# Optimization experiments

Hardware: AMD Instinct MI355X
Metric: run time of the kernel (lower is better)

The kernel has to match this reference:

```python
import jax, jax.numpy as jnp
import numpy as np

WS = 7    # window size
SS = 3    # shift size
NH = 6    # num heads
EPS = 1e-5


def _ln(x, g, b):
    m = jnp.mean(x, -1, keepdims=True)
    v = jnp.mean((x - m) ** 2, -1, keepdims=True)
    return (x - m) * jax.lax.rsqrt(v + EPS) * g + b


def _win_part(x, ws):
    # (B, H, W, C) -> (B*nW, ws*ws, C)
    B, H, W, C = x.shape
    x = x.reshape(B, H // ws, ws, W // ws, ws, C).transpose(0, 1, 3, 2, 4, 5)
    return x.reshape(-1, ws * ws, C)


def _win_rev(w, ws, B, H, W):
    # (B*nW, ws*ws, C) -> (B, H, W, C)
    C = w.shape[-1]
    x = w.reshape(B, H // ws, W // ws, ws, ws, C).transpose(0, 1, 3, 2, 4, 5)
    return x.reshape(B, H, W, C)


def _forward(x, norm1_g, norm1_b, qkv_w, qkv_b, proj_w, proj_b, norm2_g, norm2_b,
             fc1_w, fc1_b, fc2_w, fc2_b, rel_table, mask_matrix, H, W, rel_index):
    B, L, C = x.shape
    hd = C // NH
    shortcut = x
    h = _ln(x, norm1_g, norm1_b).reshape(B, H, W, C)
    pad_r = (WS - W % WS) % WS
    pad_b = (WS - H % WS) % WS
    h = jnp.pad(h, ((0, 0), (0, pad_b), (0, pad_r), (0, 0)))
    Hp, Wp = H + pad_b, W + pad_r
    # cyclic shift (shift_size > 0 path)
    h = jnp.roll(h, (-SS, -SS), axis=(1, 2))
    xw = _win_part(h, WS)                                   # [Bw, N, C]
    Bw, N, _ = xw.shape
    qkv = (xw @ qkv_w + qkv_b).reshape(Bw, N, 3, NH, hd)
    q = qkv[:, :, 0].transpose(0, 2, 1, 3) * (hd ** -0.5)   # [Bw, NH, N, hd]
    k = qkv[:, :, 1].transpose(0, 2, 1, 3)
    v = qkv[:, :, 2].transpose(0, 2, 1, 3)
    attn = q @ k.transpose(0, 1, 3, 2)                      # [Bw, NH, N, N]
    bias = rel_table[rel_index.reshape(-1)].reshape(N, N, NH).transpose(2, 0, 1)
    attn = attn + bias[None]
    nW = mask_matrix.shape[0]
    attn = attn.reshape(Bw // nW, nW, NH, N, N) + mask_matrix[None, :, None]
    attn = jax.nn.softmax(attn.reshape(Bw, NH, N, N), axis=-1)
    o = (attn @ v).transpose(0, 2, 1, 3).reshape(Bw, N, C)
    o = o @ proj_w + proj_b
    h = _win_rev(o, WS, B, Hp, Wp)
    h = jnp.roll(h, (SS, SS), axis=(1, 2))[:, :H, :W, :].reshape(B, L, C)
    x = shortcut + h
    y = _ln(x, norm2_g, norm2_b)
    y = jax.nn.gelu(y @ fc1_w + fc1_b, approximate=False) @ fc2_w + fc2_b  # torch GELU = exact erf
    return x + y


def setup_inputs() -> dict:
    B, H, W, C, HID = 32, 56, 56, 192, 768
    ws, ss = WS, SS
    ks = jax.random.split(jax.random.key(0), 8)
    rn = lambda i, shp, s: jax.random.normal(ks[i], shp, jnp.float32) * s
    inp = {
        'x': rn(0, (B, H * W, C), 1.0),
        'norm1_g': jnp.ones((C,), jnp.float32), 'norm1_b': jnp.zeros((C,), jnp.float32),
        'qkv_w': rn(1, (C, 3 * C), 0.02), 'qkv_b': jnp.zeros((3 * C,), jnp.float32),
        'proj_w': rn(2, (C, C), 0.02), 'proj_b': jnp.zeros((C,), jnp.float32),
        'norm2_g': jnp.ones((C,), jnp.float32), 'norm2_b': jnp.zeros((C,), jnp.float32),
        'fc1_w': rn(3, (C, HID), 0.02), 'fc1_b': jnp.zeros((HID,), jnp.float32),
        'fc2_w': rn(4, (HID, C), 0.02), 'fc2_b': jnp.zeros((C,), jnp.float32),
        'rel_table': rn(5, ((2 * ws - 1) ** 2, NH), 0.02),
    }
    # relative position index (same construction as torch buffer)
    coords = np.stack(np.meshgrid(np.arange(ws), np.arange(ws), indexing='ij')).reshape(2, -1)
    rel = (coords[:, :, None] - coords[:, None, :]).transpose(1, 2, 0)
    rel[..., 0] += ws - 1
    rel[..., 1] += ws - 1
    rel[..., 0] *= 2 * ws - 1
    inp['rel_index'] = jnp.asarray(rel.sum(-1), jnp.int32)  # [49, 49]
    # shifted-window attention mask (standard Swin construction)
    img = np.zeros((1, H, W, 1), np.float32)
    cnt = 0
    for hs in (slice(0, -ws), slice(-ws, -ss), slice(-ss, None)):
        for wsl in (slice(0, -ws), slice(-ws, -ss), slice(-ss, None)):
            img[:, hs, wsl, :] = cnt
            cnt += 1
    mw = img.reshape(1, H // ws, ws, W // ws, ws, 1).transpose(0, 1, 3, 2, 4, 5).reshape(-1, ws * ws)
    diff = mw[:, None, :] - mw[:, :, None]
    inp['mask_matrix'] = jnp.asarray(np.where(diff != 0, -100.0, 0.0), jnp.float32)  # [64, 49, 49]
    inp['H'] = H
    inp['W'] = W
    return inp


def reference(x, norm1_g, norm1_b, qkv_w, qkv_b, proj_w, proj_b, norm2_g, norm2_b,
              fc1_w, fc1_b, fc2_w, fc2_b, rel_table, rel_index, mask_matrix, H, W):
    return _forward(x, norm1_g, norm1_b, qkv_w, qkv_b, proj_w, proj_b, norm2_g, norm2_b,
                    fc1_w, fc1_b, fc2_w, fc2_b, rel_table, mask_matrix, H, W, rel_index)
```

## Files before the change

kernel.cpp:

```cpp
#include <hip/hip_runtime.h>

typedef __bf16 bf8 __attribute__((ext_vector_type(8)));
typedef float f4 __attribute__((ext_vector_type(4)));

__device__ __forceinline__ void stb(unsigned short* p, float v) { *(__bf16*)p = (__bf16)v; }

__device__ __forceinline__ void gl_lds16(const unsigned short* g, unsigned short* l) {
  __builtin_amdgcn_global_load_lds((const __attribute__((address_space(1))) unsigned int*)g,
                                   (__attribute__((address_space(3))) unsigned int*)l,
                                   16, 0, 0);
}

__device__ __forceinline__ float gelu_fast(float v) {
  float w = v * v;
  float u = v * (-2.30222655f - 0.10294296f * w);
  float e = __builtin_amdgcn_exp2f(u);
  return v * __builtin_amdgcn_rcpf(1.0f + e);
}

__global__ void transpose_kernel(const float* __restrict__ in,
                                 unsigned short* __restrict__ out, int K, int N) {
  int idx = blockIdx.x * 256 + threadIdx.x;
  if (idx < K * N) {
    int n = idx / K, k = idx - n * K;
    stb(&out[idx], in[k * N + n]);
  }
}

__global__ __launch_bounds__(256) void ln_kernel(const float* __restrict__ xin,
                                                 const float* __restrict__ g,
                                                 const float* __restrict__ bb,
                                                 unsigned short* __restrict__ out) {
  long token = (long)blockIdx.x * 4 + (threadIdx.x >> 6);
  int lane = threadIdx.x & 63;
  const float* row = xin + token * 192;
  float v[3] = {row[lane], row[lane + 64], row[lane + 128]};
  float s = v[0] + v[1] + v[2];
#pragma unroll
  for (int m = 1; m < 64; m <<= 1) s += __shfl_xor(s, m, 64);
  float mean = s * (1.0f / 192.0f);
  float d0 = v[0] - mean, d1 = v[1] - mean, d2 = v[2] - mean;
  float dd = d0 * d0 + d1 * d1 + d2 * d2;
#pragma unroll
  for (int m = 1; m < 64; m <<= 1) dd += __shfl_xor(dd, m, 64);
  float rstd = rsqrtf(dd * (1.0f / 192.0f) + 1e-5f);
  unsigned short* orow = out + token * 192;
#pragma unroll
  for (int i = 0; i < 3; i++) {
    int c = lane + i * 64;
    stb(&orow[c], (v[i] - mean) * rstd * g[c] + bb[c]);
  }
}

template <int EPI>
__global__ __launch_bounds__(256) void gemm_kernel(const unsigned short* __restrict__ A,
                                                   const unsigned short* __restrict__ Bt,
                                                   const float* __restrict__ bias,
                                                   const float* __restrict__ res,
                                                   void* __restrict__ out, int K, int N) {
  __shared__ __align__(16) unsigned short As[2][128 * 64];
  __shared__ __align__(16) unsigned short Bs[2][64 * 64];
  const int tid = threadIdx.x;
  const int wave = tid >> 6;
  const int lane = tid & 63;
  const int quad = lane >> 4;
  const int l16 = lane & 15;

  const int NX = gridDim.x;
  int lin = blockIdx.y * NX + blockIdx.x;
  const int T = NX * gridDim.y;
  if ((T & 7) == 0) {
    lin = (lin & 7) * (T >> 3) + (lin >> 3);
  }
  const int bx = lin % NX;
  const int by = lin / NX;
  const long m0 = (long)by * 128;
  const long n0 = (long)bx * 64;

  long a_src[4];
  int a_dstc[4];
#pragma unroll
  for (int j = 0; j < 4; ++j) {
    int L = (wave * 4 + j) * 64 + lane;
    int row = L >> 3, cs = L & 7;
    a_src[j] = (m0 + row) * (long)K + ((cs ^ (row & 7)) << 3);
    a_dstc[j] = (wave * 4 + j) * 512;
  }
  long b_src[2];
  int b_dstc[2];
#pragma unroll
  for (int j = 0; j < 2; ++j) {
    int L = (wave * 2 + j) * 64 + lane;
    int row = L >> 3, cs = L & 7;
    b_src[j] = (n0 + row) * (long)K + ((cs ^ (row & 7)) << 3);
    b_dstc[j] = (wave * 2 + j) * 512;
  }

  const int nT = K >> 6;
  f4 acc[2][4] = {};

#pragma unroll
  for (int j = 0; j < 4; ++j) gl_lds16(A + a_src[j], &As[0][a_dstc[j]]);
#pragma unroll
  for (int j = 0; j < 2; ++j) gl_lds16(Bt + b_src[j], &Bs[0][b_dstc[j]]);

  int cur = 0;
  for (int t = 0; t < nT; ++t) {
    if (t + 1 < nT) {
      const int k0 = (t + 1) << 6;
#pragma unroll
      for (int j = 0; j < 4; ++j) gl_lds16(A + a_src[j] + k0, &As[cur ^ 1][a_dstc[j]]);
#pragma unroll
      for (int j = 0; j < 2; ++j) gl_lds16(Bt + b_src[j] + k0, &Bs[cur ^ 1][b_dstc[j]]);
      asm volatile("s_waitcnt vmcnt(6)" ::: "memory");
    } else {
      asm volatile("s_waitcnt vmcnt(0)" ::: "memory");
    }
    __builtin_amdgcn_s_barrier();
    __builtin_amdgcn_sched_barrier(0);
#pragma unroll
    for (int kk = 0; kk < 2; ++kk) {
      bf8 a[2], b[4];
#pragma unroll
      for (int mt = 0; mt < 2; ++mt) {
        int r = wave * 32 + mt * 16 + l16;
        int c = kk * 4 + quad;
        a[mt] = *(const bf8*)&As[cur][r * 64 + ((c ^ (r & 7)) << 3)];
      }
#pragma unroll
      for (int nt = 0; nt < 4; ++nt) {
        int r = nt * 16 + l16;
        int c = kk * 4 + quad;
        b[nt] = *(const bf8*)&Bs[cur][r * 64 + ((c ^ (r & 7)) << 3)];
      }
#pragma unroll
      for (int mt = 0; mt < 2; ++mt)
#pragma unroll
        for (int nt = 0; nt < 4; ++nt)
          acc[mt][nt] = __builtin_amdgcn_mfma_f32_16x16x32_bf16(a[mt], b[nt], acc[mt][nt], 0, 0, 0);
    }
    __builtin_amdgcn_sched_barrier(0);
    __builtin_amdgcn_s_barrier();
    cur ^= 1;
  }

#pragma unroll
  for (int nt = 0; nt < 4; ++nt) {
    long n = n0 + nt * 16 + l16;
    float bv = bias[n];
#pragma unroll
    for (int mt = 0; mt < 2; ++mt) {
#pragma unroll
      for (int r = 0; r < 4; ++r) {
        long m = m0 + wave * 32 + mt * 16 + quad * 4 + r;
        float v = acc[mt][nt][r] + bv;
        long idx = m * N + n;
        if (EPI == 0) {
          stb(&((unsigned short*)out)[idx], v);
        } else if (EPI == 2) {
          stb(&((unsigned short*)out)[idx], gelu_fast(v));
        } else {
          ((float*)out)[idx] = v + res[idx];
        }
      }
    }
  }
}

__global__ __launch_bounds__(256) void proj_ln_kernel(const unsigned short* __restrict__ A,
                                                      const unsigned short* __restrict__ Bt,
                                                      const float* __restrict__ bias,
                                                      const float* __restrict__ res,
                                                      const float* __restrict__ g2,
                                                      const float* __restrict__ b2,
                                                      float* __restrict__ xres,
                                                      unsigned short* __restrict__ lnout) {
  __shared__ __align__(16) unsigned short As[2][128 * 64];
  __shared__ __align__(16) unsigned short Bs[2][192 * 64];
  const int tid = threadIdx.x;
  const int wave = tid >> 6;
  const int lane = tid & 63;
  const int quad = lane >> 4;
  const int l16 = lane & 15;

  int lin = blockIdx.y;
  const int T = gridDim.y;
  if ((T & 7) == 0) lin = (lin & 7) * (T >> 3) + (lin >> 3);
  const long m0 = (long)lin * 128;

  long a_src[4];
  int a_dstc[4];
#pragma unroll
  for (int j = 0; j < 4; ++j) {
    int L = (wave * 4 + j) * 64 + lane;
    int row = L >> 3, cs = L & 7;
    a_src[j] = (m0 + row) * 192L + ((cs ^ (row & 7)) << 3);
    a_dstc[j] = (wave * 4 + j) * 512;
  }
  long b_src[6];
  int b_dstc[6];
#pragma unroll
  for (int j = 0; j < 6; ++j) {
    int L = (wave * 6 + j) * 64 + lane;
    int row = L >> 3, cs = L & 7;
    b_src[j] = row * 192L + ((cs ^ (row & 7)) << 3);
    b_dstc[j] = (wave * 6 + j) * 512;
  }

  f4 acc[2][12] = {};

#pragma unroll
  for (int j = 0; j < 4; ++j) gl_lds16(A + a_src[j], &As[0][a_dstc[j]]);
#pragma unroll
  for (int j = 0; j < 6; ++j) gl_lds16(Bt + b_src[j], &Bs[0][b_dstc[j]]);

  int cur = 0;
  for (int t = 0; t < 3; ++t) {
    if (t + 1 < 3) {
      const int k0 = (t + 1) << 6;
#pragma unroll
      for (int j = 0; j < 4; ++j) gl_lds16(A + a_src[j] + k0, &As[cur ^ 1][a_dstc[j]]);
#pragma unroll
      for (int j = 0; j < 6; ++j) gl_lds16(Bt + b_src[j] + k0, &Bs[cur ^ 1][b_dstc[j]]);
      asm volatile("s_waitcnt vmcnt(10)" ::: "memory");
    } else {
      asm volatile("s_waitcnt vmcnt(0)" ::: "memory");
    }
    __builtin_amdgcn_s_barrier();
    __builtin_amdgcn_sched_barrier(0);
#pragma unroll
    for (int kk = 0; kk < 2; ++kk) {
      bf8 a[2];
#pragma unroll
      for (int mt = 0; mt < 2; ++mt) {
        int r = wave * 32 + mt * 16 + l16;
        int c = kk * 4 + quad;
        a[mt] = *(const bf8*)&As[cur][r * 64 + ((c ^ (r & 7)) << 3)];
      }
#pragma unroll
      for (int nt = 0; nt < 12; ++nt) {
        int r = nt * 16 + l16;
        int c = kk * 4 + quad;
        bf8 b = *(const bf8*)&Bs[cur][r * 64 + ((c ^ (r & 7)) << 3)];
#pragma unroll
        for (int mt = 0; mt < 2; ++mt)
          acc[mt][nt] = __builtin_amdgcn_mfma_f32_16x16x32_bf16(a[mt], b, acc[mt][nt], 0, 0, 0);
      }
    }
    __builtin_amdgcn_sched_barrier(0);
    __builtin_amdgcn_s_barrier();
    cur ^= 1;
  }

#pragma unroll
  for (int mt = 0; mt < 2; ++mt) {
#pragma unroll
    for (int r = 0; r < 4; ++r) {
      long mm = m0 + wave * 32 + mt * 16 + quad * 4 + r;
      const float* rrow = res + mm * 192;
      float v[12];
      float s = 0.0f;
#pragma unroll
      for (int nt = 0; nt < 12; ++nt) {
        int n = nt * 16 + l16;
        float t = acc[mt][nt][r] + bias[n] + rrow[n];
        v[nt] = t;
        s += t;
      }
#pragma unroll
      for (int m = 1; m < 16; m <<= 1) s += __shfl_xor(s, m, 64);
      float mean = s * (1.0f / 192.0f);
      float d = 0.0f;
#pragma unroll
      for (int nt = 0; nt < 12; ++nt) {
        float dd = v[nt] - mean;
        d += dd * dd;
      }
#pragma unroll
      for (int m = 1; m < 16; m <<= 1) d += __shfl_xor(d, m, 64);
      float rstd = rsqrtf(d * (1.0f / 192.0f) + 1e-5f);
      float* xrow = xres + mm * 192;
      unsigned short* lrow = lnout + mm * 192;
#pragma unroll
      for (int nt = 0; nt < 12; ++nt) {
        int n = nt * 16 + l16;
        xrow[n] = v[nt];
        stb(&lrow[n], (v[nt] - mean) * rstd * g2[n] + b2[n]);
      }
    }
  }
}

__global__ __launch_bounds__(512) void mlp_kernel(const unsigned short* __restrict__ A,
                                                  const unsigned short* __restrict__ W1t,
                                                  const unsigned short* __restrict__ W2t,
                                                  const float* __restrict__ b1,
                                                  const float* __restrict__ b2,
                                                  const float* __restrict__ res,
                                                  float* __restrict__ out) {
  __shared__ __align__(16) unsigned short As[128 * 192];
  __shared__ __align__(16) unsigned short Bs[2][192 * 64];
  __shared__ __align__(16) unsigned short Gs[8][16 * 200];
  const int tid = threadIdx.x;
  const int wave = tid >> 6;
  const int lane = tid & 63;
  const int quad = lane >> 4;
  const int l16 = lane & 15;

  int lin = blockIdx.x;
  const int T = gridDim.x;
  if ((T & 7) == 0) lin = (lin & 7) * (T >> 3) + (lin >> 3);
  const long m0 = (long)lin * 128;

#pragma unroll
  for (int j = 0; j < 6; ++j) {
    int L = (wave * 6 + j) * 64 + lane;
    int row = L / 24;
    int cs = L - row * 24;
    long src = (m0 + row) * 192L + ((cs ^ (row & 7)) << 3);
    gl_lds16(A + src, &As[(wave * 6 + j) * 512]);
  }

  int brow[3], bswz[3];
#pragma unroll
  for (int j = 0; j < 3; ++j) {
    int L = (wave * 3 + j) * 64 + lane;
    brow[j] = L >> 3;
    int cs = L & 7;
    bswz[j] = ((cs ^ (brow[j] & 7)) << 3);
  }

#define STAGE_B(c_, p_, kb_, buf_)                                            \
  {                                                                           \
    _Pragma("unroll") for (int j = 0; j < 3; ++j) {                           \
      long src_;                                                              \
      if (p_ == 0)                                                            \
        src_ = (long)(c_) * 36864 + (long)brow[j] * 192 + (kb_) * 64 + bswz[j]; \
      else                                                                    \
        src_ = (long)brow[j] * 768 + (c_) * 192 + (kb_) * 64 + bswz[j];       \
      gl_lds16(((p_) == 0 ? W1t : W2t) + src_, &Bs[buf_][(wave * 3 + j) * 512]); \
    }                                                                         \
  }

  f4 oacc[12] = {};

  STAGE_B(0, 0, 0, 0);

  int cur = 0;
  const int myrowA = (wave * 16 + l16) * 192;
  const int swzl = l16 & 7;
  unsigned short* Gmy = &Gs[wave][0];

#pragma unroll 1
  for (int c = 0; c < 4; ++c) {
    f4 gacc[12] = {};
#pragma unroll 1
    for (int kb = 0; kb < 3; ++kb) {
      if (kb < 2) {
        STAGE_B(c, 0, kb + 1, cur ^ 1);
      } else {
        STAGE_B(c, 1, 0, cur ^ 1);
      }
      asm volatile("s_waitcnt vmcnt(3)" ::: "memory");
      __builtin_amdgcn_s_barrier();
      __builtin_amdgcn_sched_barrier(0);
#pragma unroll
      for (int kk = 0; kk < 2; ++kk) {
        int csr = (kb * 2 + kk) * 4 + quad;
        bf8 a = *(const bf8*)&As[myrowA + ((csr ^ swzl) << 3)];
#pragma unroll
        for (int nt = 0; nt < 12; ++nt) {
          bf8 b = *(const bf8*)&Bs[cur][(nt * 16 + l16) * 64 + (((kk * 4 + quad) ^ swzl) << 3)];
          gacc[nt] = __builtin_amdgcn_mfma_f32_16x16x32_bf16(a, b, gacc[nt], 0, 0, 0);
        }
      }
      __builtin_amdgcn_sched_barrier(0);
      __builtin_amdgcn_s_barrier();
      cur ^= 1;
    }
#pragma unroll
    for (int nt = 0; nt < 12; ++nt) {
      float bv = b1[c * 192 + nt * 16 + l16];
#pragma unroll
      for (int r = 0; r < 4; ++r) {
        float g = gelu_fast(gacc[nt][r] + bv);
        stb(&Gmy[(quad * 4 + r) * 200 + nt * 16 + l16], g);
      }
    }
    asm volatile("s_waitcnt lgkmcnt(0)" ::: "memory");
    __builtin_amdgcn_sched_barrier(0);
#pragma unroll 1
    for (int kb = 0; kb < 3; ++kb) {
      if (kb < 2) {
        STAGE_B(c, 1, kb + 1, cur ^ 1);
        asm volatile("s_waitcnt vmcnt(3)" ::: "memory");
      } else if (c < 3) {
        STAGE_B(c + 1, 0, 0, cur ^ 1);
        asm volatile("s_waitcnt vmcnt(3)" ::: "memory");
      } else {
        asm volatile("s_waitcnt vmcnt(0)" ::: "memory");
      }
      __builtin_amdgcn_s_barrier();
      __builtin_amdgcn_sched_barrier(0);
#pragma unroll
      for (int kk = 0; kk < 2; ++kk) {
        bf8 a = *(const bf8*)&Gmy[l16 * 200 + (kb * 2 + kk) * 32 + quad * 8];
#pragma unroll
        for (int nt = 0; nt < 12; ++nt) {
          bf8 b = *(const bf8*)&Bs[cur][(nt * 16 + l16) * 64 + (((kk * 4 + quad) ^ swzl) << 3)];
          oacc[nt] = __builtin_amdgcn_mfma_f32_16x16x32_bf16(a, b, oacc[nt], 0, 0, 0);
        }
      }
      __builtin_amdgcn_sched_barrier(0);
      __builtin_amdgcn_s_barrier();
      cur ^= 1;
    }
  }
#undef STAGE_B

#pragma unroll
  for (int r = 0; r < 4; ++r) {
    long mm = m0 + wave * 16 + quad * 4 + r;
    const float* rrow = res + mm * 192;
    float* orow = out + mm * 192;
#pragma unroll
    for (int nt = 0; nt < 12; ++nt) {
      int n = nt * 16 + l16;
      orow[n] = oacc[nt][r] + b2[n] + rrow[n];
    }
  }
}

__global__ __launch_bounds__(128) void attn_kernel(const unsigned short* __restrict__ qkv,
                                                   const float* __restrict__ rel_t,
                                                   unsigned short* __restrict__ o) {
  __shared__ __align__(16) unsigned short sh[2 * 6912];
  __shared__ float relh[2][170];
  __shared__ int toksh[2][49];
  __shared__ int zsh[2][49];
  const int wave = threadIdx.x >> 6;
  const int lane = threadIdx.x & 63;
  const int quad = lane >> 4;
  const int l16 = lane & 15;
  const int p = blockIdx.x * 2 + wave;
  const int head = p % 6;
  const int wib = p / 6;
  const int wi = wib & 63;
  const int b = wib >> 6;
  unsigned short* Vts = sh + wave * 6912;
  unsigned short* Ps = Vts + 2304;

  if (lane < 49) {
    int r = lane / 7, c = lane - (lane / 7) * 7;
    int ph = (wi >> 3) * 7 + r, pw = (wi & 7) * 7 + c;
    int h = ph + 3; if (h >= 56) h -= 56;
    int w = pw + 3; if (w >= 56) w -= 56;
    toksh[wave][lane] = (b * 56 + h) * 56 + w;
    int zh = (ph < 49) ? 0 : (ph < 53 ? 1 : 2);
    int zw = (pw < 49) ? 0 : (pw < 53 ? 1 : 2);
    zsh[wave][lane] = zh * 3 + zw;
  }
  for (int i = lane; i < 169; i += 64) relh[wave][i] = rel_t[i * 6 + head];
  {
#pragma unroll
    for (int e = 0; e < 4; e++) {
      int ee = lane + e * 64;
      int d = ee >> 3, c8 = ee & 7;
      *(unsigned int*)&Vts[d * 72 + 48 + c8 * 2] = 0u;
    }
  }
  __syncthreads();

  for (int e = lane; e < 196; e += 64) {
    int n = e >> 2, c = e & 3;
    int t = toksh[wave][n];
    uint4 vc = *(const uint4*)(qkv + (long)t * 576 + head * 32 + 384 + c * 8);
    const unsigned short* vv = (const unsigned short*)&vc;
#pragma unroll
    for (int j = 0; j < 8; j++) Vts[(c * 8 + j) * 72 + n] = vv[j];
  }

  bf8 zv;
#pragma unroll
  for (int q8 = 0; q8 < 8; q8++) zv[q8] = (__bf16)0.0f;
  bf8 af[4], bf_[4];
#pragma unroll
  for (int i = 0; i < 4; i++) {
    int row = 16 * i + l16;
    int rv = row < 49 ? row : 48;
    long base = (long)toksh[wave][rv] * 576 + head * 32 + quad * 8;
    bf8 qf = *(const bf8*)(qkv + base);
    bf8 kf = *(const bf8*)(qkv + base + 192);
    if (row >= 49) { qf = zv; kf = zv; }
    af[i] = qf;
    bf_[i] = kf;
  }

  f4 S[4][4];
#pragma unroll
  for (int i = 0; i < 4; i++)
#pragma unroll
    for (int j = 0; j < 4; j++)
      S[i][j] = __builtin_amdgcn_mfma_f32_16x16x32_bf16(af[i], bf_[j], (f4){0.f, 0.f, 0.f, 0.f}, 0, 0, 0);

  int colv[4], colkey[4], zcol[4];
#pragma unroll
  for (int jt = 0; jt < 4; jt++) {
    int col = 16 * jt + l16;
    int cc = col < 49 ? col : 48;
    int rj = cc / 7, cj = cc - rj * 7;
    colkey[jt] = rj * 13 + cj;
    zcol[jt] = zsh[wave][cc];
    colv[jt] = (col < 49);
  }

  __syncthreads();

  const float sc = 0.17677669529663687f;
#pragma unroll
  for (int it = 0; it < 4; it++) {
#pragma unroll
    for (int r = 0; r < 4; r++) {
      int row = 16 * it + quad * 4 + r;
      int row2 = row < 49 ? row : 48;
      int ri = row2 / 7, ci = row2 - ri * 7;
      int rk = ri * 13 + ci + 84;
      int zr = zsh[wave][row2];
      float v[4];
#pragma unroll
      for (int jt = 0; jt < 4; jt++) {
        float bias = relh[wave][rk - colkey[jt]];
        float msk = (zr == zcol[jt]) ? 0.0f : -100.0f;
        float val = S[it][jt][r] * sc + bias + msk;
        v[jt] = colv[jt] ? val : -1e30f;
      }
      float mx = fmaxf(fmaxf(v[0], v[1]), fmaxf(v[2], v[3]));
#pragma unroll
      for (int m = 1; m < 16; m <<= 1) mx = fmaxf(mx, __shfl_xor(mx, m, 64));
      float e0 = __expf(v[0] - mx), e1 = __expf(v[1] - mx), e2 = __expf(v[2] - mx), e3 = __expf(v[3] - mx);
      float sum = e0 + e1 + e2 + e3;
#pragma unroll
      for (int m = 1; m < 16; m <<= 1) sum += __shfl_xor(sum, m, 64);
      float inv = 1.0f / sum;
      stb(&Ps[row * 72 + 0 + l16], e0 * inv);
      stb(&Ps[row * 72 + 16 + l16], e1 * inv);
      stb(&Ps[row * 72 + 32 + l16], e2 * inv);
      stb(&Ps[row * 72 + 48 + l16], e3 * inv);
    }
  }
  __syncthreads();

  f4 O[4][2] = {};
#pragma unroll
  for (int ks = 0; ks < 2; ks++) {
    bf8 pv[2];
#pragma unroll
    for (int nt = 0; nt < 2; nt++) pv[nt] = *(const bf8*)&Vts[(16 * nt + l16) * 72 + ks * 32 + quad * 8];
#pragma unroll
    for (int mt = 0; mt < 4; mt++) {
      bf8 pa = *(const bf8*)&Ps[(16 * mt + l16) * 72 + ks * 32 + quad * 8];
#pragma unroll
      for (int nt = 0; nt < 2; nt++)
        O[mt][nt] = __builtin_amdgcn_mfma_f32_16x16x32_bf16(pa, pv[nt], O[mt][nt], 0, 0, 0);
    }
  }
#pragma unroll
  for (int mt = 0; mt < 4; mt++) {
#pragma unroll
    for (int r = 0; r < 4; r++) {
      int row = 16 * mt + quad * 4 + r;
      if (row < 49) {
        long base = (long)toksh[wave][row] * 192 + head * 32 + l16;
        stb(&o[base], O[mt][0][r]);
        stb(&o[base + 16], O[mt][1][r]);
      }
    }
  }
}

extern "C" void kernel_launch(void* const* d_in, const int* in_sizes, int n_in,
                              void* d_out, int out_size, void* d_ws, size_t ws_size,
                              hipStream_t stream) {
  const float* x      = (const float*)d_in[0];
  const float* n1g    = (const float*)d_in[1];
  const float* n1b    = (const float*)d_in[2];
  const float* qkv_w  = (const float*)d_in[3];
  const float* qkv_b  = (const float*)d_in[4];
  const float* proj_w = (const float*)d_in[5];
  const float* proj_b = (const float*)d_in[6];
  const float* n2g    = (const float*)d_in[7];
  const float* n2b    = (const float*)d_in[8];
  const float* fc1_w  = (const float*)d_in[9];
  const float* fc1_b  = (const float*)d_in[10];
  const float* fc2_w  = (const float*)d_in[11];
  const float* fc2_b  = (const float*)d_in[12];
  const float* rel_t  = (const float*)d_in[13];
  const float* mask   = (const float*)d_in[15];
  (void)mask;

  char* ws = (char*)d_ws;
  unsigned short* qkv_wT  = (unsigned short*)(ws + 0);
  unsigned short* proj_wT = (unsigned short*)(ws + 221184);
  unsigned short* fc1_wT  = (unsigned short*)(ws + 294912);
  unsigned short* fc2_wT  = (unsigned short*)(ws + 589824);
  unsigned short* bufA    = (unsigned short*)(ws + 884736);
  unsigned short* bufB    = (unsigned short*)(ws + 39419904ULL);
  float*          xres    = (float*)(ws + 193560576ULL);

  const int M = 100352;

  transpose_kernel<<<(192 * 576 + 255) / 256, 256, 0, stream>>>(qkv_w, qkv_wT, 192, 576);
  transpose_kernel<<<(192 * 192 + 255) / 256, 256, 0, stream>>>(proj_w, proj_wT, 192, 192);
  transpose_kernel<<<(192 * 768 + 255) / 256, 256, 0, stream>>>(fc1_w, fc1_wT, 192, 768);
  transpose_kernel<<<(768 * 192 + 255) / 256, 256, 0, stream>>>(fc2_w, fc2_wT, 768, 192);

  ln_kernel<<<M / 4, 256, 0, stream>>>(x, n1g, n1b, bufA);
  gemm_kernel<0><<<dim3(576 / 64, M / 128), 256, 0, stream>>>(bufA, qkv_wT, qkv_b, nullptr, bufB, 192, 576);
  attn_kernel<<<12288 / 2, 128, 0, stream>>>(bufB, rel_t, bufA);
  proj_ln_kernel<<<dim3(1, M / 128), 256, 0, stream>>>(bufA, proj_wT, proj_b, x, n2g, n2b, xres, bufA);
  mlp_kernel<<<M / 128, 512, 0, stream>>>(bufA, fc1_wT, fc2_wT, fc1_b, fc2_b, xres, (float*)d_out);
}
```

Baseline: 490.1 us.

## Shrink MLP blocks to 64 rows, hold A in registers, single-buffer weights

The fused MLP kernel moves from 128-row, 512-thread blocks to 64-row, 256-thread blocks. The A tile now sits in per-wave registers instead of LDS, and the weight tile is staged through registers into one LDS buffer rather than double-buffered with direct global-to-LDS loads. LDS use per block drops sharply and launch bounds ask for 3 blocks per CU, to raise occupancy. In exchange, each block does less work per weight load, so weight traffic doubles. The single buffer also needs an extra barrier and a full vmcnt wait each step, which can expose load latency.

Measured after the change: 733.3 us. +49.6%, slower.

```diff
diff --git a/kernel.cpp b/kernel.cpp
--- a/kernel.cpp
+++ b/kernel.cpp
@@ -291,16 +291,15 @@
   }
 }
 
-__global__ __launch_bounds__(512) void mlp_kernel(const unsigned short* __restrict__ A,
-                                                  const unsigned short* __restrict__ W1t,
-                                                  const unsigned short* __restrict__ W2t,
-                                                  const float* __restrict__ b1,
-                                                  const float* __restrict__ b2,
-                                                  const float* __restrict__ res,
-                                                  float* __restrict__ out) {
-  __shared__ __align__(16) unsigned short As[128 * 192];
-  __shared__ __align__(16) unsigned short Bs[2][192 * 64];
-  __shared__ __align__(16) unsigned short Gs[8][16 * 200];
+__global__ __launch_bounds__(256, 3) void mlp_kernel(const unsigned short* __restrict__ A,
+                                                     const unsigned short* __restrict__ W1t,
+                                                     const unsigned short* __restrict__ W2t,
+                                                     const float* __restrict__ b1,
+                                                     const float* __restrict__ b2,
+                                                     const float* __restrict__ res,
+                                                     float* __restrict__ out) {
+  __shared__ __align__(16) unsigned short Bs[192 * 64];
+  __shared__ __align__(16) unsigned short Gs[4][16 * 200];
   const int tid = threadIdx.x;
   const int wave = tid >> 6;
   const int lane = tid & 63;
@@ -310,73 +309,68 @@
   int lin = blockIdx.x;
   const int T = gridDim.x;
   if ((T & 7) == 0) lin = (lin & 7) * (T >> 3) + (lin >> 3);
-  const long m0 = (long)lin * 128;
-
-#pragma unroll
-  for (int j = 0; j < 6; ++j) {
-    int L = (wave * 6 + j) * 64 + lane;
-    int row = L / 24;
-    int cs = L - row * 24;
-    long src = (m0 + row) * 192L + ((cs ^ (row & 7)) << 3);
-    gl_lds16(A + src, &As[(wave * 6 + j) * 512]);
-  }
-
-  int brow[3], bswz[3];
-#pragma unroll
-  for (int j = 0; j < 3; ++j) {
-    int L = (wave * 3 + j) * 64 + lane;
-    brow[j] = L >> 3;
-    int cs = L & 7;
-    bswz[j] = ((cs ^ (brow[j] & 7)) << 3);
-  }
-
-#define STAGE_B(c_, p_, kb_, buf_)                                            \
-  {                                                                           \
-    _Pragma("unroll") for (int j = 0; j < 3; ++j) {                           \
-      long src_;                                                              \
-      if (p_ == 0)                                                            \
-        src_ = (long)(c_) * 36864 + (long)brow[j] * 192 + (kb_) * 64 + bswz[j]; \
-      else                                                                    \
-        src_ = (long)brow[j] * 768 + (c_) * 192 + (kb_) * 64 + bswz[j];       \
-      gl_lds16(((p_) == 0 ? W1t : W2t) + src_, &Bs[buf_][(wave * 3 + j) * 512]); \
-    }                                                                         \
+  const long m0 = (long)lin * 64;
+
+  const long arow = (m0 + wave * 16 + l16) * 192 + quad * 8;
+  bf8 afrag[6];
+#pragma unroll
+  for (int s = 0; s < 6; ++s) afrag[s] = *(const bf8*)(A + arow + s * 32);
+
+  uint4 breg[6];
+#define BLOAD(c_, p_, kb_)                                                      \
+  {                                                                             \
+    _Pragma("unroll") for (int j = 0; j < 6; ++j) {                             \
+      int L = j * 256 + tid;                                                    \
+      int row = L >> 3, cs = L & 7;                                             \
+      long src_;                                                                \
+      if ((p_) == 0)                                                            \
+        src_ = ((long)(c_) * 192 + row) * 192 + (kb_) * 64 + ((cs ^ (row & 7)) << 3); \
+      else                                                                      \
+        src_ = (long)row * 768 + (c_) * 192 + (kb_) * 64 + ((cs ^ (row & 7)) << 3);   \
+      breg[j] = *(const uint4*)(((p_) == 0 ? W1t : W2t) + src_);                \
+    }                                                                           \
+  }
+#define BWRITE()                                                                \
+  {                                                                             \
+    _Pragma("unroll") for (int j = 0; j < 6; ++j) {                             \
+      int L = j * 256 + tid;                                                    \
+      *(uint4*)&Bs[L * 8] = breg[j];                                            \
+    }                                                                           \
   }
 
   f4 oacc[12] = {};
-
-  STAGE_B(0, 0, 0, 0);
-
-  int cur = 0;
-  const int myrowA = (wave * 16 + l16) * 192;
   const int swzl = l16 & 7;
   unsigned short* Gmy = &Gs[wave][0];
+
+  BLOAD(0, 0, 0);
+  asm volatile("s_waitcnt vmcnt(0)" ::: "memory");
+  BWRITE();
+  asm volatile("s_waitcnt lgkmcnt(0)" ::: "memory");
+  __builtin_amdgcn_s_barrier();
+  __builtin_amdgcn_sched_barrier(0);
 
 #pragma unroll 1
   for (int c = 0; c < 4; ++c) {
     f4 gacc[12] = {};
 #pragma unroll 1
     for (int kb = 0; kb < 3; ++kb) {
-      if (kb < 2) {
-        STAGE_B(c, 0, kb + 1, cur ^ 1);
-      } else {
-        STAGE_B(c, 1, 0, cur ^ 1);
-      }
-      asm volatile("s_waitcnt vmcnt(3)" ::: "memory");
+      if (kb < 2) { BLOAD(c, 0, kb + 1); } else { BLOAD(c, 1, 0); }
+#pragma unroll
+      for (int kk = 0; kk < 2; ++kk) {
+        bf8 a = afrag[kb * 2 + kk];
+#pragma unroll
+        for (int nt = 0; nt < 12; ++nt) {
+          bf8 b = *(const bf8*)&Bs[(nt * 16 + l16) * 64 + (((kk * 4 + quad) ^ swzl) << 3)];
+          gacc[nt] = __builtin_amdgcn_mfma_f32_16x16x32_bf16(a, b, gacc[nt], 0, 0, 0);
+        }
+      }
+      __builtin_amdgcn_sched_barrier(0);
+      __builtin_amdgcn_s_barrier();
+      asm volatile("s_waitcnt vmcnt(0)" ::: "memory");
+      BWRITE();
+      asm volatile("s_waitcnt lgkmcnt(0)" ::: "memory");
       __builtin_amdgcn_s_barrier();
       __builtin_amdgcn_sched_barrier(0);
-#pragma unroll
-      for (int kk = 0; kk < 2; ++kk) {
-        int csr = (kb * 2 + kk) * 4 + quad;
-        bf8 a = *(const bf8*)&As[myrowA + ((csr ^ swzl) << 3)];
-#pragma unroll
-        for (int nt = 0; nt < 12; ++nt) {
-          bf8 b = *(const bf8*)&Bs[cur][(nt * 16 + l16) * 64 + (((kk * 4 + quad) ^ swzl) << 3)];
-          gacc[nt] = __builtin_amdgcn_mfma_f32_16x16x32_bf16(a, b, gacc[nt], 0, 0, 0);
-        }
-      }
-      __builtin_amdgcn_sched_barrier(0);
-      __builtin_amdgcn_s_barrier();
-      cur ^= 1;
     }
 #pragma unroll
     for (int nt = 0; nt < 12; ++nt) {
@@ -391,32 +385,31 @@
     __builtin_amdgcn_sched_barrier(0);
 #pragma unroll 1
     for (int kb = 0; kb < 3; ++kb) {
-      if (kb < 2) {
-        STAGE_B(c, 1, kb + 1, cur ^ 1);
-        asm volatile("s_waitcnt vmcnt(3)" ::: "memory");
-      } else if (c < 3) {
-        STAGE_B(c + 1, 0, 0, cur ^ 1);
-        asm volatile("s_waitcnt vmcnt(3)" ::: "memory");
-      } else {
+      const bool has_next = (kb < 2) || (c < 3);
+      if (kb < 2) { BLOAD(c, 1, kb + 1); }
+      else if (c < 3) { BLOAD(c + 1, 0, 0); }
+#pragma unroll
+      for (int kk = 0; kk < 2; ++kk) {
+        bf8 a = *(const bf8*)&Gmy[l16 * 200 + (kb * 2 + kk) * 32 + quad * 8];
+#pragma unroll
+        for (int nt = 0; nt < 12; ++nt) {
+          bf8 b = *(const bf8*)&Bs[(nt * 16 + l16) * 64 + (((kk * 4 + quad) ^ swzl) << 3)];
+          oacc[nt] = __builtin_amdgcn_mfma_f32_16x16x32_bf16(a, b, oacc[nt], 0, 0, 0);
+        }
+      }
+      __builtin_amdgcn_sched_barrier(0);
+      __builtin_amdgcn_s_barrier();
+      if (has_next) {
         asm volatile("s_waitcnt vmcnt(0)" ::: "memory");
+        BWRITE();
+        asm volatile("s_waitcnt lgkmcnt(0)" ::: "memory");
       }
       __builtin_amdgcn_s_barrier();
       __builtin_amdgcn_sched_barrier(0);
-#pragma unroll
-      for (int kk = 0; kk < 2; ++kk) {
-        bf8 a = *(const bf8*)&Gmy[l16 * 200 + (kb * 2 + kk) * 32 + quad * 8];
-#pragma unroll
-        for (int nt = 0; nt < 12; ++nt) {
-          bf8 b = *(const bf8*)&Bs[cur][(nt * 16 + l16) * 64 + (((kk * 4 + quad) ^ swzl) << 3)];
-          oacc[nt] = __builtin_amdgcn_mfma_f32_16x16x32_bf16(a, b, oacc[nt], 0, 0, 0);
-        }
-      }
-      __builtin_amdgcn_sched_barrier(0);
-      __builtin_amdgcn_s_barrier();
-      cur ^= 1;
-    }
-  }
-#undef STAGE_B
+    }
+  }
+#undef BLOAD
+#undef BWRITE
 
 #pragma unroll
   for (int r = 0; r < 4; ++r) {
@@ -618,5 +611,5 @@
   gemm_kernel<0><<<dim3(576 / 64, M / 128), 256, 0, stream>>>(bufA, qkv_wT, qkv_b, nullptr, bufB, 192, 576);
   attn_kernel<<<12288 / 2, 128, 0, stream>>>(bufB, rel_t, bufA);
   proj_ln_kernel<<<dim3(1, M / 128), 256, 0, stream>>>(bufA, proj_wT, proj_b, x, n2g, n2b, xres, bufA);
-  mlp_kernel<<<M / 128, 512, 0, stream>>>(bufA, fc1_wT, fc2_wT, fc1_b, fc2_b, xres, (float*)d_out);
-}
+  mlp_kernel<<<M / 64, 256, 0, stream>>>(bufA, fc1_wT, fc2_wT, fc1_b, fc2_b, xres, (float*)d_out);
+}
```
